# Optimization experiments

Hardware: AMD Instinct MI355X
Metric: run time of the kernel (lower is better)

The kernel has to match this reference:

```python
import jax, jax.numpy as jnp
from jax import lax
import numpy as np

SNN_STEPS = 15
BETA = 0.9
THR = 1.0
SLOPE = 25.0  # snntorch fast_sigmoid default slope

@jax.custom_vjp
def spike(x):
    return (x > 0).astype(x.dtype)

def _spike_fwd(x):
    return (x > 0).astype(x.dtype), x

def _spike_bwd(x, g):
    return (g / (SLOPE * jnp.abs(x) + 1.0) ** 2,)

spike.defvjp(_spike_fwd, _spike_bwd)


def setup_inputs() -> dict:
    key = jax.random.key(0)
    ks = jax.random.split(key, 16)
    B, C, H, S, A, Hd, Rh = 256, 20, 10, 64, 16, 128, 64

    def w(k, shape):
        fan_in = shape[0]
        return jax.random.normal(k, shape, jnp.float32) / jnp.sqrt(jnp.float32(fan_in))

    return {
        "current_state": jax.random.normal(ks[0], (B, S), jnp.float32),
        "actions": jax.random.normal(ks[1], (C, B, H, A), jnp.float32),
        "noise": jax.random.normal(ks[2], (C, B, H, S), jnp.float32),
        "Wse": w(ks[3], (S, Hd)), "bse": jnp.zeros((Hd,), jnp.float32),
        "Wae": w(ks[4], (A, Hd)), "bae": jnp.zeros((Hd,), jnp.float32),
        "W1": w(ks[5], (2 * Hd, Hd)), "b1": jnp.zeros((Hd,), jnp.float32),
        "W2": w(ks[6], (Hd, Hd)), "b2": jnp.zeros((Hd,), jnp.float32),
        "Wdec": w(ks[7], (Hd, S)), "bdec": jnp.zeros((S,), jnp.float32),
        "Wunc": w(ks[8], (Hd, S)), "bunc": jnp.zeros((S,), jnp.float32),
        "Wr1": w(ks[9], (S + A, Rh)), "br1": jnp.zeros((Rh,), jnp.float32),
        "Wr2": w(ks[10], (Rh, Rh)), "br2": jnp.zeros((Rh,), jnp.float32),
        "Wr3": w(ks[11], (Rh, 1)), "br3": jnp.zeros((1,), jnp.float32),
    }


def _plan(current_state, actions, noise, Wse, bse, Wae, bae, W1, b1, W2, b2,
          Wdec, bdec, Wunc, bunc, Wr1, br1, Wr2, br2, Wr3, br3):
    C, B, H, A = actions.shape
    S = current_state.shape[-1]
    CB = C * B
    # fold candidates into batch -> fully vectorized Monte Carlo rollouts
    state0 = jnp.broadcast_to(current_state[None], (C, B, S)).reshape(CB, S)
    acts = actions.transpose(2, 0, 1, 3).reshape(H, CB, A)   # [H, CB, A]
    noi = noise.transpose(2, 0, 1, 3).reshape(H, CB, S)      # [H, CB, S]

    def world_step(state, act_t, noise_t):
        se = jax.nn.relu(state @ Wse + bse)
        ae = jax.nn.relu(act_t @ Wae + bae)
        cur = jnp.concatenate([se, ae], axis=-1) @ W1 + b1   # constant over snn steps

        def snn_step(carry, _):
            mem1, mem2 = carry
            # snntorch Leaky (reset-by-subtraction, reset uses previous spike)
            mem1 = BETA * mem1 + cur - THR * spike(mem1 - THR)
            spk1 = spike(mem1 - THR)
            cur2 = spk1 @ W2 + b2
            mem2 = BETA * mem2 + cur2 - THR * spike(mem2 - THR)
            return (mem1, mem2), None

        zeros = jnp.zeros_like(cur)
        (_, mem2), _ = lax.scan(snn_step, (zeros, zeros), None, length=SNN_STEPS)
        mean = mem2 @ Wdec + bdec
        var = jax.nn.softplus(mem2 @ Wunc + bunc)
        return mean + noise_t * jnp.sqrt(var + 1e-8)  # sample_next_state

    def rollout(state, xs):
        act_t, noise_t = xs
        ns = world_step(state, act_t, noise_t)
        return ns, ns

    _, states = lax.scan(rollout, state0, (acts, noi))       # [H, CB, S]

    # reward model over all (state, action) pairs at once
    x = jnp.concatenate([states, acts], axis=-1)             # [H, CB, S+A]
    h = jax.nn.relu(x @ Wr1 + br1)
    h = jax.nn.relu(h @ Wr2 + br2)
    r = (h @ Wr3 + br3)[..., 0]                              # [H, CB]
    cum = r.sum(axis=0).reshape(C, B).T                      # [B, C]

    best_idx = jnp.argmax(cum, axis=1)                       # [B]
    best_value = jnp.take_along_axis(cum, best_idx[:, None], axis=1)[:, 0]
    best_actions = actions[best_idx, jnp.arange(B)]          # [B, H, A]
    return best_actions, best_value


def reference(current_state, actions, noise, Wse, bse, Wae, bae, W1, b1, W2, b2,
              Wdec, bdec, Wunc, bunc, Wr1, br1, Wr2, br2, Wr3, br3):
    return _plan(current_state, actions, noise, Wse, bse, Wae, bae, W1, b1, W2, b2,
                 Wdec, bdec, Wunc, bunc, Wr1, br1, Wr2, br2, Wr3, br3)


if __name__ == "__main__":
    out = reference(**setup_inputs())
    print(out[0].shape, out[1].shape)
```

## Files before the change

kernel.cpp:

```cpp
#include <hip/hip_runtime.h>
#include <math.h>

#define CC 20
#define BB 256
#define HH 10
#define SS 64
#define AA 16
#define HD 128
#define RH 64
#define CBR (CC*BB)
#define NSNN 15

__device__ __forceinline__ float softplus_np(float u) {
    if (u > 0.0f) {
        float ef = (float)exp((double)(-u));
        float l1 = (float)log1p((double)ef);
        return __fadd_rn(u, l1);
    } else if (u < 0.0f) {
        float ef = (float)exp((double)u);
        return (float)log1p((double)ef);
    } else {
        return 0.69314718055994530942f;
    }
}

__global__ __launch_bounds__(128) void world_kernel(
    int h,
    const float* __restrict__ current_state,
    const float* __restrict__ actions,
    const float* __restrict__ noise,
    const float* __restrict__ Wse, const float* __restrict__ bse,
    const float* __restrict__ Wae, const float* __restrict__ bae,
    const float* __restrict__ W1,  const float* __restrict__ b1,
    const float* __restrict__ W2,  const float* __restrict__ b2,
    const float* __restrict__ Wdec, const float* __restrict__ bdec,
    const float* __restrict__ Wunc, const float* __restrict__ bunc,
    float* __restrict__ states)
{
    const int cb = blockIdx.x;
    const int j  = threadIdx.x;

    __shared__ float    s_state[SS];
    __shared__ float    s_sae[2*HD];
    __shared__ unsigned s_mask[HD];
    __shared__ float    s_mem2[HD];
    __shared__ float    s_mu[2*SS];

    if (j < SS) {
        s_state[j] = (h == 0) ? current_state[(size_t)(cb % BB)*SS + j]
                              : states[((size_t)(h-1)*CBR + cb)*SS + j];
    }
    __syncthreads();

    float acc = 0.0f;
    for (int i = 0; i < SS; i++)
        acc = fmaf(s_state[i], Wse[i*HD + j], acc);
    float se = fmaxf(__fadd_rn(acc, bse[j]), 0.0f);

    const float* act = actions + ((size_t)cb*HH + h)*AA;
    acc = 0.0f;
    for (int i = 0; i < AA; i++)
        acc = fmaf(act[i], Wae[i*HD + j], acc);
    float ae = fmaxf(__fadd_rn(acc, bae[j]), 0.0f);

    s_sae[j]      = se;
    s_sae[HD + j] = ae;
    __syncthreads();

    acc = 0.0f;
    for (int i = 0; i < 2*HD; i++)
        acc = fmaf(s_sae[i], W1[i*HD + j], acc);
    const float cur = __fadd_rn(acc, b1[j]);

    unsigned mask = 0u;
    float m1 = 0.0f;
    #pragma unroll
    for (int t = 0; t < NSNN; t++) {
        float sp1old = (__fsub_rn(m1, 1.0f) > 0.0f) ? 1.0f : 0.0f;
        m1 = __fsub_rn(__fadd_rn(__fmul_rn(0.9f, m1), cur), sp1old);
        if (__fsub_rn(m1, 1.0f) > 0.0f) mask |= (1u << t);
    }
    s_mask[j] = mask;
    __syncthreads();

    const int lane = j & 63;
    unsigned mlo = s_mask[lane];
    unsigned mhi = s_mask[64 + lane];

    float cur2[NSNN];
    #pragma unroll
    for (int t = 0; t < NSNN; t++) cur2[t] = 0.0f;

    const float* W2j = W2 + j;
    #pragma unroll 1
    for (int k = 0; k < 64; k++) {
        float w = W2j[(size_t)k * HD];
        unsigned m = (unsigned)__builtin_amdgcn_readlane((int)mlo, k);
        if (m == 0u) continue;
        #pragma unroll
        for (int t = 0; t < NSNN; t++) {
            float sv = __uint_as_float(((m >> t) & 1u) * 0x3f800000u);
            cur2[t] = fmaf(sv, w, cur2[t]);
        }
    }
    #pragma unroll 1
    for (int k = 0; k < 64; k++) {
        float w = W2j[(size_t)(64 + k) * HD];
        unsigned m = (unsigned)__builtin_amdgcn_readlane((int)mhi, k);
        if (m == 0u) continue;
        #pragma unroll
        for (int t = 0; t < NSNN; t++) {
            float sv = __uint_as_float(((m >> t) & 1u) * 0x3f800000u);
            cur2[t] = fmaf(sv, w, cur2[t]);
        }
    }

    const float b2j = b2[j];
    float m2 = 0.0f;
    #pragma unroll
    for (int t = 0; t < NSNN; t++) {
        float c2 = __fadd_rn(cur2[t], b2j);
        float sp2old = (__fsub_rn(m2, 1.0f) > 0.0f) ? 1.0f : 0.0f;
        m2 = __fsub_rn(__fadd_rn(__fmul_rn(0.9f, m2), c2), sp2old);
    }
    s_mem2[j] = m2;
    __syncthreads();

    {
        const float* W    = (j < SS) ? Wdec : Wunc;
        const float* bias = (j < SS) ? bdec : bunc;
        int o = j & (SS - 1);
        float c = 0.0f;
        for (int n = 0; n < HD; n++)
            c = fmaf(s_mem2[n], W[n*SS + o], c);
        s_mu[j] = __fadd_rn(c, bias[o]);
    }
    __syncthreads();

    if (j < SS) {
        float mean = s_mu[j];
        float u    = s_mu[SS + j];
        float var  = softplus_np(u);
        float sv   = sqrtf(__fadd_rn(var, 1e-8f));
        float nz   = noise[((size_t)cb*HH + h)*SS + j];
        states[((size_t)h*CBR + cb)*SS + j] = __fadd_rn(mean, __fmul_rn(nz, sv));
    }
}

__global__ __launch_bounds__(64) void reward_kernel(
    const float* __restrict__ states,
    const float* __restrict__ actions,
    const float* __restrict__ Wr1, const float* __restrict__ br1,
    const float* __restrict__ Wr2, const float* __restrict__ br2,
    const float* __restrict__ Wr3, const float* __restrict__ br3,
    float* __restrict__ cum)
{
    const int cb = blockIdx.x;
    const int j  = threadIdx.x;
    __shared__ float s_x[SS + AA];
    __shared__ float s_h[RH];
    __shared__ float s_h2[RH];

    float total = 0.0f;
    for (int h = 0; h < HH; h++) {
        __syncthreads();
        s_x[j] = states[((size_t)h*CBR + cb)*SS + j];
        if (j < AA) s_x[SS + j] = actions[((size_t)cb*HH + h)*AA + j];
        __syncthreads();

        float a = 0.0f;
        for (int i = 0; i < SS + AA; i++)
            a = fmaf(s_x[i], Wr1[i*RH + j], a);
        s_h[j] = fmaxf(__fadd_rn(a, br1[j]), 0.0f);
        __syncthreads();

        float g = 0.0f;
        for (int i = 0; i < RH; i++)
            g = fmaf(s_h[i], Wr2[i*RH + j], g);
        s_h2[j] = fmaxf(__fadd_rn(g, br2[j]), 0.0f);
        __syncthreads();

        if (j == 0) {
            float r = 0.0f;
            for (int k = 0; k < RH; k++)
                r = fmaf(s_h2[k], Wr3[k], r);
            r = __fadd_rn(r, br3[0]);
            total = __fadd_rn(total, r);
        }
    }
    if (j == 0) cum[cb] = total;
}

__global__ __launch_bounds__(64) void select_kernel(
    const float* __restrict__ cum,
    const float* __restrict__ actions,
    float* __restrict__ out)
{
    const int b = blockIdx.x;
    const int j = threadIdx.x;
    __shared__ int s_c;

    if (j == 0) {
        float best = cum[b];
        int bc = 0;
        for (int c = 1; c < CC; c++) {
            float v = cum[(size_t)c*BB + b];
            if (v > best) { best = v; bc = c; }
        }
        s_c = bc;
        out[(size_t)BB*HH*AA + b] = best;
    }
    __syncthreads();
    const int bc = s_c;
    const float* src = actions + ((size_t)bc*BB + b)*HH*AA;
    for (int i = j; i < HH*AA; i += 64) out[(size_t)b*HH*AA + i] = src[i];
}

extern "C" void kernel_launch(void* const* d_in, const int* in_sizes, int n_in,
                              void* d_out, int out_size, void* d_ws, size_t ws_size,
                              hipStream_t stream)
{
    const float* current_state = (const float*)d_in[0];
    const float* actions = (const float*)d_in[1];
    const float* noise   = (const float*)d_in[2];
    const float* Wse = (const float*)d_in[3];
    const float* bse = (const float*)d_in[4];
    const float* Wae = (const float*)d_in[5];
    const float* bae = (const float*)d_in[6];
    const float* W1  = (const float*)d_in[7];
    const float* b1  = (const float*)d_in[8];
    const float* W2  = (const float*)d_in[9];
    const float* b2  = (const float*)d_in[10];
    const float* Wdec = (const float*)d_in[11];
    const float* bdec = (const float*)d_in[12];
    const float* Wunc = (const float*)d_in[13];
    const float* bunc = (const float*)d_in[14];
    const float* Wr1 = (const float*)d_in[15];
    const float* br1 = (const float*)d_in[16];
    const float* Wr2 = (const float*)d_in[17];
    const float* br2 = (const float*)d_in[18];
    const float* Wr3 = (const float*)d_in[19];
    const float* br3 = (const float*)d_in[20];

    float* states = (float*)d_ws;
    float* cum    = states + (size_t)HH*CBR*SS;

    for (int h = 0; h < HH; h++) {
        world_kernel<<<CBR, HD, 0, stream>>>(h, current_state, actions, noise,
            Wse, bse, Wae, bae, W1, b1, W2, b2, Wdec, bdec, Wunc, bunc, states);
    }
    reward_kernel<<<CBR, RH, 0, stream>>>(states, actions, Wr1, br1, Wr2, br2, Wr3, br3, cum);
    select_kernel<<<BB, 64, 0, stream>>>(cum, actions, (float*)d_out);
}
```

Baseline: 848.1 us.

## Process two rollouts per block in world kernel to reuse weight loads

Each world_kernel block now handles two candidate rollouts instead of one, so every weight element loaded from global memory (Wse, Wae, W1, W2, Wdec/Wunc) is used for two accumulations. Shared buffers are interleaved per rollout and read as float2. This halves the number of blocks and the weight traffic per rollout. In exchange it uses more registers (two 15-element cur2 arrays) and exposes fewer blocks for parallelism.

```diff
diff --git a/kernel.cpp b/kernel.cpp
--- a/kernel.cpp
+++ b/kernel.cpp
@@ -10,6 +10,7 @@
 #define RH 64
 #define CBR (CC*BB)
 #define NSNN 15
+#define RT 2
 
 __device__ __forceinline__ float softplus_np(float u) {
     if (u > 0.0f) {
@@ -37,113 +38,171 @@
     const float* __restrict__ Wunc, const float* __restrict__ bunc,
     float* __restrict__ states)
 {
-    const int cb = blockIdx.x;
-    const int j  = threadIdx.x;
-
-    __shared__ float    s_state[SS];
-    __shared__ float    s_sae[2*HD];
-    __shared__ unsigned s_mask[HD];
-    __shared__ float    s_mem2[HD];
-    __shared__ float    s_mu[2*SS];
+    const int cb0 = blockIdx.x * RT;
+    const int j   = threadIdx.x;
+
+    __shared__ float    s_state[SS][RT];
+    __shared__ float    s_sae[2*HD][RT];
+    __shared__ unsigned s_mask[HD][RT];
+    __shared__ float    s_mem2[HD][RT];
+    __shared__ float    s_mu[2*SS][RT];
 
     if (j < SS) {
-        s_state[j] = (h == 0) ? current_state[(size_t)(cb % BB)*SS + j]
-                              : states[((size_t)(h-1)*CBR + cb)*SS + j];
-    }
-    __syncthreads();
-
-    float acc = 0.0f;
-    for (int i = 0; i < SS; i++)
-        acc = fmaf(s_state[i], Wse[i*HD + j], acc);
-    float se = fmaxf(__fadd_rn(acc, bse[j]), 0.0f);
-
-    const float* act = actions + ((size_t)cb*HH + h)*AA;
-    acc = 0.0f;
-    for (int i = 0; i < AA; i++)
-        acc = fmaf(act[i], Wae[i*HD + j], acc);
-    float ae = fmaxf(__fadd_rn(acc, bae[j]), 0.0f);
-
-    s_sae[j]      = se;
-    s_sae[HD + j] = ae;
-    __syncthreads();
-
-    acc = 0.0f;
-    for (int i = 0; i < 2*HD; i++)
-        acc = fmaf(s_sae[i], W1[i*HD + j], acc);
-    const float cur = __fadd_rn(acc, b1[j]);
-
-    unsigned mask = 0u;
-    float m1 = 0.0f;
+        #pragma unroll
+        for (int r = 0; r < RT; r++) {
+            int cb = cb0 + r;
+            s_state[j][r] = (h == 0) ? current_state[(size_t)(cb % BB)*SS + j]
+                                     : states[((size_t)(h-1)*CBR + cb)*SS + j];
+        }
+    }
+    __syncthreads();
+
+    float a0 = 0.0f, a1 = 0.0f;
+    for (int i = 0; i < SS; i++) {
+        float w = Wse[i*HD + j];
+        float2 st = *(const float2*)&s_state[i][0];
+        a0 = fmaf(st.x, w, a0);
+        a1 = fmaf(st.y, w, a1);
+    }
+    float se0 = fmaxf(__fadd_rn(a0, bse[j]), 0.0f);
+    float se1 = fmaxf(__fadd_rn(a1, bse[j]), 0.0f);
+
+    const float* act0 = actions + ((size_t)(cb0+0)*HH + h)*AA;
+    const float* act1 = actions + ((size_t)(cb0+1)*HH + h)*AA;
+    a0 = 0.0f; a1 = 0.0f;
+    for (int i = 0; i < AA; i++) {
+        float w = Wae[i*HD + j];
+        a0 = fmaf(act0[i], w, a0);
+        a1 = fmaf(act1[i], w, a1);
+    }
+    float ae0 = fmaxf(__fadd_rn(a0, bae[j]), 0.0f);
+    float ae1 = fmaxf(__fadd_rn(a1, bae[j]), 0.0f);
+
+    s_sae[j][0]      = se0;  s_sae[j][1]      = se1;
+    s_sae[HD + j][0] = ae0;  s_sae[HD + j][1] = ae1;
+    __syncthreads();
+
+    a0 = 0.0f; a1 = 0.0f;
+    for (int i = 0; i < 2*HD; i++) {
+        float w = W1[i*HD + j];
+        float2 sv = *(const float2*)&s_sae[i][0];
+        a0 = fmaf(sv.x, w, a0);
+        a1 = fmaf(sv.y, w, a1);
+    }
+    const float cur0 = __fadd_rn(a0, b1[j]);
+    const float cur1 = __fadd_rn(a1, b1[j]);
+
+    unsigned mask0 = 0u, mask1 = 0u;
+    {
+        float m1a = 0.0f, m1b = 0.0f;
+        #pragma unroll
+        for (int t = 0; t < NSNN; t++) {
+            float spa = (__fsub_rn(m1a, 1.0f) > 0.0f) ? 1.0f : 0.0f;
+            m1a = __fsub_rn(__fadd_rn(__fmul_rn(0.9f, m1a), cur0), spa);
+            if (__fsub_rn(m1a, 1.0f) > 0.0f) mask0 |= (1u << t);
+            float spb = (__fsub_rn(m1b, 1.0f) > 0.0f) ? 1.0f : 0.0f;
+            m1b = __fsub_rn(__fadd_rn(__fmul_rn(0.9f, m1b), cur1), spb);
+            if (__fsub_rn(m1b, 1.0f) > 0.0f) mask1 |= (1u << t);
+        }
+    }
+    s_mask[j][0] = mask0;
+    s_mask[j][1] = mask1;
+    __syncthreads();
+
+    const int lane = j & 63;
+    unsigned mlo0 = s_mask[lane][0],      mlo1 = s_mask[lane][1];
+    unsigned mhi0 = s_mask[64 + lane][0], mhi1 = s_mask[64 + lane][1];
+
+    float c20[NSNN], c21[NSNN];
     #pragma unroll
-    for (int t = 0; t < NSNN; t++) {
-        float sp1old = (__fsub_rn(m1, 1.0f) > 0.0f) ? 1.0f : 0.0f;
-        m1 = __fsub_rn(__fadd_rn(__fmul_rn(0.9f, m1), cur), sp1old);
-        if (__fsub_rn(m1, 1.0f) > 0.0f) mask |= (1u << t);
-    }
-    s_mask[j] = mask;
-    __syncthreads();
-
-    const int lane = j & 63;
-    unsigned mlo = s_mask[lane];
-    unsigned mhi = s_mask[64 + lane];
-
-    float cur2[NSNN];
-    #pragma unroll
-    for (int t = 0; t < NSNN; t++) cur2[t] = 0.0f;
+    for (int t = 0; t < NSNN; t++) { c20[t] = 0.0f; c21[t] = 0.0f; }
 
     const float* W2j = W2 + j;
     #pragma unroll 1
     for (int k = 0; k < 64; k++) {
         float w = W2j[(size_t)k * HD];
-        unsigned m = (unsigned)__builtin_amdgcn_readlane((int)mlo, k);
-        if (m == 0u) continue;
-        #pragma unroll
-        for (int t = 0; t < NSNN; t++) {
-            float sv = __uint_as_float(((m >> t) & 1u) * 0x3f800000u);
-            cur2[t] = fmaf(sv, w, cur2[t]);
+        unsigned m0 = (unsigned)__builtin_amdgcn_readlane((int)mlo0, k);
+        unsigned m1 = (unsigned)__builtin_amdgcn_readlane((int)mlo1, k);
+        if (m0) {
+            #pragma unroll
+            for (int t = 0; t < NSNN; t++) {
+                float sv = __uint_as_float(((m0 >> t) & 1u) * 0x3f800000u);
+                c20[t] = fmaf(sv, w, c20[t]);
+            }
+        }
+        if (m1) {
+            #pragma unroll
+            for (int t = 0; t < NSNN; t++) {
+                float sv = __uint_as_float(((m1 >> t) & 1u) * 0x3f800000u);
+                c21[t] = fmaf(sv, w, c21[t]);
+            }
         }
     }
     #pragma unroll 1
     for (int k = 0; k < 64; k++) {
         float w = W2j[(size_t)(64 + k) * HD];
-        unsigned m = (unsigned)__builtin_amdgcn_readlane((int)mhi, k);
-        if (m == 0u) continue;
+        unsigned m0 = (unsigned)__builtin_amdgcn_readlane((int)mhi0, k);
+        unsigned m1 = (unsigned)__builtin_amdgcn_readlane((int)mhi1, k);
+        if (m0) {
+            #pragma unroll
+            for (int t = 0; t < NSNN; t++) {
+                float sv = __uint_as_float(((m0 >> t) & 1u) * 0x3f800000u);
+                c20[t] = fmaf(sv, w, c20[t]);
+            }
+        }
+        if (m1) {
+            #pragma unroll
+            for (int t = 0; t < NSNN; t++) {
+                float sv = __uint_as_float(((m1 >> t) & 1u) * 0x3f800000u);
+                c21[t] = fmaf(sv, w, c21[t]);
+            }
+        }
+    }
+
+    const float b2j = b2[j];
+    {
+        float m2a = 0.0f, m2b = 0.0f;
         #pragma unroll
         for (int t = 0; t < NSNN; t++) {
-            float sv = __uint_as_float(((m >> t) & 1u) * 0x3f800000u);
-            cur2[t] = fmaf(sv, w, cur2[t]);
-        }
-    }
-
-    const float b2j = b2[j];
-    float m2 = 0.0f;
-    #pragma unroll
-    for (int t = 0; t < NSNN; t++) {
-        float c2 = __fadd_rn(cur2[t], b2j);
-        float sp2old = (__fsub_rn(m2, 1.0f) > 0.0f) ? 1.0f : 0.0f;
-        m2 = __fsub_rn(__fadd_rn(__fmul_rn(0.9f, m2), c2), sp2old);
-    }
-    s_mem2[j] = m2;
+            float ca = __fadd_rn(c20[t], b2j);
+            float spa = (__fsub_rn(m2a, 1.0f) > 0.0f) ? 1.0f : 0.0f;
+            m2a = __fsub_rn(__fadd_rn(__fmul_rn(0.9f, m2a), ca), spa);
+            float cb_ = __fadd_rn(c21[t], b2j);
+            float spb = (__fsub_rn(m2b, 1.0f) > 0.0f) ? 1.0f : 0.0f;
+            m2b = __fsub_rn(__fadd_rn(__fmul_rn(0.9f, m2b), cb_), spb);
+        }
+        s_mem2[j][0] = m2a;
+        s_mem2[j][1] = m2b;
+    }
     __syncthreads();
 
     {
         const float* W    = (j < SS) ? Wdec : Wunc;
         const float* bias = (j < SS) ? bdec : bunc;
         int o = j & (SS - 1);
-        float c = 0.0f;
-        for (int n = 0; n < HD; n++)
-            c = fmaf(s_mem2[n], W[n*SS + o], c);
-        s_mu[j] = __fadd_rn(c, bias[o]);
+        float c0 = 0.0f, c1 = 0.0f;
+        for (int n = 0; n < HD; n++) {
+            float w = W[n*SS + o];
+            float2 m2v = *(const float2*)&s_mem2[n][0];
+            c0 = fmaf(m2v.x, w, c0);
+            c1 = fmaf(m2v.y, w, c1);
+        }
+        s_mu[j][0] = __fadd_rn(c0, bias[o]);
+        s_mu[j][1] = __fadd_rn(c1, bias[o]);
     }
     __syncthreads();
 
     if (j < SS) {
-        float mean = s_mu[j];
-        float u    = s_mu[SS + j];
-        float var  = softplus_np(u);
-        float sv   = sqrtf(__fadd_rn(var, 1e-8f));
-        float nz   = noise[((size_t)cb*HH + h)*SS + j];
-        states[((size_t)h*CBR + cb)*SS + j] = __fadd_rn(mean, __fmul_rn(nz, sv));
+        #pragma unroll
+        for (int r = 0; r < RT; r++) {
+            int cb = cb0 + r;
+            float mean = s_mu[j][r];
+            float u    = s_mu[SS + j][r];
+            float var  = softplus_np(u);
+            float sv   = sqrtf(__fadd_rn(var, 1e-8f));
+            float nz   = noise[((size_t)cb*HH + h)*SS + j];
+            states[((size_t)h*CBR + cb)*SS + j] = __fadd_rn(mean, __fmul_rn(nz, sv));
+        }
     }
 }
 
@@ -246,7 +305,7 @@
     float* cum    = states + (size_t)HH*CBR*SS;
 
     for (int h = 0; h < HH; h++) {
-        world_kernel<<<CBR, HD, 0, stream>>>(h, current_state, actions, noise,
+        world_kernel<<<CBR/RT, HD, 0, stream>>>(h, current_state, actions, noise,
             Wse, bse, Wae, bae, W1, b1, W2, b2, Wdec, bdec, Wunc, bunc, states);
     }
     reward_kernel<<<CBR, RH, 0, stream>>>(states, actions, Wr1, br1, Wr2, br2, Wr3, br3, cum);
```

Measured after the change: 934.8 us. +10.2%, slower.
